# Kernel optimization log

Measured on AMD Instinct MI355X. Metric: run time of the kernel, lower is better.

## Reference

```python
import jax, jax.numpy as jnp
import numpy as np

L = 8192   # sequence length
B = 4      # batch
D = 512    # embed_dim
NDIM = 16  # EMA state dim
Z = 128    # shared q/k dim
W = 128    # attention window
MP = 256   # max relative positions
NEG = -50000.0  # TOKEN_SELF_ATTN_VALUE-style mask fill


def setup_inputs() -> dict:
    key = jax.random.key(0)
    ks = jax.random.split(key, 16)
    def tn(k, shp, std):  # truncated-normal-ish init (clipped normal)
        return jnp.clip(jax.random.normal(k, shp) * std, -2 * std, 2 * std)
    val = jnp.ones((NDIM, 1)).at[1::2].set(-1.0)  # MultiHeadEMA beta init pattern
    return {
        "x": jax.random.normal(ks[0], (L, B, D), dtype=jnp.float32),
        "delta": tn(ks[1], (D, NDIM, 1), 0.2),
        "alpha": tn(ks[2], (D, NDIM, 1), 0.2),
        "beta": tn(ks[3], (D, NDIM, 1), 0.02) + val,
        "gamma": jax.random.normal(ks[4], (D, NDIM)),
        "omega": jax.random.normal(ks[5], (D,)),
        "Wp": tn(ks[6], (D, 1), 0.02),      # LatentConfigurator weight_proj
        "bp": jnp.zeros((1,)),
        "temp": jnp.array([0.5 * np.log(D)], dtype=jnp.float32),  # log(sqrt(D))
        "Wz": tn(ks[7], (D, Z), 0.02),
        "qg": jax.random.normal(ks[8], (Z,)) * 0.02 + 1.0,
        "qb": jnp.zeros((Z,)),
        "kg": jax.random.normal(ks[9], (Z,)) * 0.02 + 1.0,
        "kb": jnp.zeros((Z,)),
        "Wv": tn(ks[10], (D, D), 0.02),
        "relb": tn(ks[11], (2 * MP - 1,), 0.02),  # FastRelativePositionalBias table
    }


def _rotary(t, cos, sin):
    # t: (B, L, Z); cos/sin: (L, Z//2). Complex rotation on interleaved pairs.
    t1, t2 = t[..., 0::2], t[..., 1::2]
    return jnp.stack([t1 * cos - t2 * sin, t1 * sin + t2 * cos], axis=-1).reshape(t.shape)


def _forward(x, delta, alpha, beta, gamma, omega, Wp, bp, temp, Wz, qg, qb, kg, kb, Wv, relb):
    scale = 1.0 / np.sqrt(NDIM)
    # ---- MultiHeadEMA: damped EMA as long convolution via FFT ----
    p = jax.nn.sigmoid(delta)                      # (D,N,1)
    a = jax.nn.sigmoid(alpha)
    logq = jnp.log1p(-(p * a))                     # log(1 - p*alpha)
    t = jnp.arange(L, dtype=jnp.float32)
    kern = (p * beta) * jnp.exp(logq * t)          # (D,N,L) Vandermonde kernel
    k1d = jnp.einsum('dnl,dn->dl', kern, gamma * scale)  # (D,L)
    xb = x.transpose(1, 2, 0)                      # (B,D,L)
    conv = jnp.fft.irfft(jnp.fft.rfft(xb, n=2 * L) * jnp.fft.rfft(k1d, n=2 * L), n=2 * L)[..., :L]
    mx = jax.nn.silu(conv.transpose(2, 0, 1) + x * omega)  # (L,B,D)
    # ---- LatentConfigurator: sigmoid token routing (proj_dim==1) ----
    pi = jax.nn.sigmoid((mx @ Wp + bp) / jnp.exp(temp))[..., 0].T  # (B,L)
    mxb = mx.transpose(1, 0, 2)                    # (B,L,D)
    sel = pi > 0.5
    idx = jnp.cumsum(sel.astype(jnp.int32), axis=1) * sel  # (B,L); 0 -> dropped slot
    counts = sel.sum(axis=1)                       # (B,)
    bi = jnp.arange(B)[:, None]
    # compress_seq: scatter selected tokens to compact prefix (slot 0 dropped)
    c = jnp.zeros((B, L + 1, D), mx.dtype).at[bi, idx].add(mxb * sel[..., None])[:, 1:]
    # ---- windowed attention over compressed tokens ----
    z = jax.nn.silu(c @ Wz)                        # (B,L,Z)
    freqs = 1.0 / (10000.0 ** (jnp.arange(0, Z, 2, dtype=jnp.float32) / Z))
    ang = jnp.arange(L, dtype=jnp.float32)[:, None] * freqs
    cos, sin = jnp.cos(ang), jnp.sin(ang)
    q = _rotary(z * qg + qb, cos, sin)
    kk = _rotary(z * kg + kb, cos, sin)
    v = jax.nn.silu(c @ Wv)                        # (B,L,D)
    n = L // W
    qw = q.reshape(B, n, W, Z)
    def look_around(tw):  # prepend previous window: (B,n,W,f) -> (B,n,2W,f)
        prev = jnp.pad(tw, ((0, 0), (1, 0), (0, 0), (0, 0)))[:, :-1]
        return jnp.concatenate([prev, tw], axis=2)
    kw = look_around(kk.reshape(B, n, W, Z))
    vw = look_around(v.reshape(B, n, W, D))
    base = (jnp.arange(n) * W)[:, None, None]
    qabs = base + jnp.arange(W)[None, :, None]         # (n,W,1)
    kabs = base + jnp.arange(-W, W)[None, None, :]     # (n,1,2W)
    mask = (kabs <= qabs) & (kabs >= 0) & (kabs[None] < counts[:, None, None, None])  # (B,n,W,2W)
    rel = jnp.arange(-W, W)[None, :] - jnp.arange(W)[:, None]   # (W,2W)
    bias = relb[jnp.clip(rel + MP - 1, 0, 2 * MP - 2)]          # (W,2W)
    scores = jnp.einsum('bnwz,bnkz->bnwk', qw, kw) / np.sqrt(Z) + bias
    attn = jax.nn.softmax(jnp.where(mask, scores, NEG), axis=-1)
    h = jnp.einsum('bnwk,bnkd->bnwd', attn, vw).reshape(B, L, D)
    # ---- extract: gather back to original positions, gate by pi ----
    hpad = jnp.concatenate([jnp.zeros((B, 1, D), h.dtype), h], axis=1)
    hsel = jnp.take_along_axis(hpad, idx[..., None], axis=1)    # (B,L,D)
    return x + (hsel * pi[..., None]).transpose(1, 0, 2)        # (L,B,D)


def reference(x, delta, alpha, beta, gamma, omega, Wp, bp, temp, Wz, qg, qb, kg, kb, Wv, relb):
    return _forward(x, delta, alpha, beta, gamma, omega, Wp, bp, temp, Wz, qg, qb, kg, kb, Wv, relb)
```

## Files before the change

### kernel.cpp

```cpp
#include <hip/hip_runtime.h>
#include <math.h>

constexpr int L = 8192;
constexpr int B = 4;
constexpr int D = 512;
constexpr int NDIM = 16;
constexpr int Z = 128;
constexpr float NEGF = -50000.0f;
constexpr int CCL = 64;
constexpr int NCH = L / CCL;
constexpr int FMAX = 64;

typedef short s16x8 __attribute__((ext_vector_type(8)));
typedef float f32x4 __attribute__((ext_vector_type(4)));

typedef __attribute__((address_space(1))) const void* as1cv;
typedef __attribute__((address_space(3))) void* as3v;

__device__ __forceinline__ void gld16(const void* g, void* l) {
  __builtin_amdgcn_global_load_lds((as1cv)g, (as3v)l, 16, 0, 0);
}

__device__ __forceinline__ unsigned short f2bf(float f) {
  unsigned u = __builtin_bit_cast(unsigned, f);
  u += 0x7fffu + ((u >> 16) & 1u);
  return (unsigned short)(u >> 16);
}

#define DPPADD(acc, ctrl, rmask)                                                   \
  {                                                                                \
    int _mv = __builtin_amdgcn_update_dpp(0, __builtin_bit_cast(int, acc),         \
                                          ctrl, rmask, 0xf, false);                \
    acc += __builtin_bit_cast(float, _mv);                                         \
  }

__global__ __launch_bounds__(256) void k_prep(const float* __restrict__ delta,
                                              const float* __restrict__ alpha,
                                              const float* __restrict__ beta,
                                              const float* __restrict__ gamma,
                                              double* __restrict__ qdn,
                                              double* __restrict__ cdn,
                                              double* __restrict__ rp1,
                                              double* __restrict__ rp2,
                                              float* __restrict__ qf,
                                              float* __restrict__ cf,
                                              float* __restrict__ r1f,
                                              float* __restrict__ r2f,
                                              int* __restrict__ fcnt) {
  int i = blockIdx.x * 256 + threadIdx.x;
  if (i == 0) *fcnt = 0;
  if (i >= D * NDIM) return;
  double p = 1.0 / (1.0 + exp(-(double)delta[i]));
  double a = 1.0 / (1.0 + exp(-(double)alpha[i]));
  double q = 1.0 - p * a;
  double c = p * (double)beta[i] * (double)gamma[i] * 0.25;
  qdn[i] = q; cdn[i] = c;
  double q2 = q * q, q4 = q2 * q2, q8 = q4 * q4;
  double q16 = q8 * q8, q32 = q16 * q16, q64 = q32 * q32;
  rp1[i] = q64;
  rp2[i] = q64 * q64;
  qf[i] = (float)q; cf[i] = (float)c;
  r1f[i] = (float)q64; r2f[i] = (float)(q64 * q64);
}

__global__ __launch_bounds__(256) void k_tab(float2* __restrict__ tab) {
  int tid = blockIdx.x * 256 + threadIdx.x;
  int i = tid & 63, j = tid >> 6;
  double freq = exp(((double)(-2 * i) / 128.0) * log(10000.0));
  float angf = (float)j * (float)freq;
  double sa, ca;
  sincos((double)angf, &sa, &ca);
  float2 r; r.x = (float)ca; r.y = (float)sa;
  tab[tid] = r;
}

__global__ __launch_bounds__(256) void k_convA(const float* __restrict__ x,
                                               const float* __restrict__ qf,
                                               float* __restrict__ E) {
  int bx = blockIdx.x;
  int tile = bx & 31, dg = (bx >> 5) & 7, b = bx >> 8;
  int dl = threadIdx.x & 63, cl = threadIdx.x >> 6;
  int dgl = dg * 64 + dl;
  int t = tile * 4 + cl;
  float q[NDIM], s[NDIM];
#pragma unroll
  for (int n = 0; n < NDIM; ++n) { q[n] = qf[dgl * NDIM + n]; s[n] = 0.f; }
  const float* xp = x + ((size_t)(t * CCL) * B + b) * D + dgl;
#pragma unroll 4
  for (int i = 0; i < CCL; ++i) {
    float xv = xp[i * (B * D)];
#pragma unroll
    for (int n = 0; n < NDIM; ++n) s[n] = fmaf(q[n], s[n], xv);
  }
  float* eb = E + ((size_t)(b * NCH + t) * NDIM) * 512 + dgl;
#pragma unroll
  for (int n = 0; n < NDIM; ++n) eb[(size_t)n * 512] = s[n];
}

__global__ __launch_bounds__(256) void k_convC(const float* __restrict__ x,
                                               const float* __restrict__ omega,
                                               const float* __restrict__ qf,
                                               const float* __restrict__ cf,
                                               const float* __restrict__ r1f,
                                               const float* __restrict__ r2f,
                                               const float* __restrict__ E,
                                               const float* __restrict__ Wp,
                                               unsigned short* __restrict__ mxb,
                                               float* __restrict__ pdot) {
  int bx = blockIdx.x;
  int tile = bx & 31, dg = (bx >> 5) & 7, b = bx >> 8;
  int dl = threadIdx.x & 63, cl = threadIdx.x >> 6;
  int dgl = dg * 64 + dl;
  int t = tile * 4 + cl;
  float q[NDIM], c[NDIM], s[NDIM];
#pragma unroll
  for (int n = 0; n < NDIM; ++n) {
    q[n] = qf[dgl * NDIM + n];
    c[n] = cf[dgl * NDIM + n];
    s[n] = 0.f;
  }
  if (t >= 1) {
    const float* e1 = E + ((size_t)(b * NCH + t - 1) * NDIM) * 512 + dgl;
#pragma unroll
    for (int n = 0; n < NDIM; ++n) s[n] = e1[(size_t)n * 512];
  }
  if (t >= 2) {
    const float* e2 = E + ((size_t)(b * NCH + t - 2) * NDIM) * 512 + dgl;
#pragma unroll
    for (int n = 0; n < NDIM; ++n) s[n] = fmaf(r1f[dgl * NDIM + n], e2[(size_t)n * 512], s[n]);
  }
  if (t >= 3) {
    const float* e3 = E + ((size_t)(b * NCH + t - 3) * NDIM) * 512 + dgl;
#pragma unroll
    for (int n = 0; n < NDIM; ++n) s[n] = fmaf(r2f[dgl * NDIM + n], e3[(size_t)n * 512], s[n]);
  }
  float om = omega[dgl];
  float wp = Wp[dgl];
  const float* xp = x + ((size_t)(t * CCL) * B + b) * D + dgl;
  unsigned short* mp = mxb + ((size_t)b * L + t * CCL) * 512 + dgl;
  float* pp = pdot + ((size_t)(b * L + t * CCL)) * 8 + dg;
#pragma unroll 4
  for (int i = 0; i < CCL; ++i) {
    float xv = xp[i * (B * D)];
#pragma unroll
    for (int n = 0; n < NDIM; ++n) s[n] = fmaf(q[n], s[n], xv);
    float p0 = c[0] * s[0], p1 = c[1] * s[1], p2 = c[2] * s[2], p3 = c[3] * s[3];
    p0 = fmaf(c[4], s[4], p0);  p1 = fmaf(c[5], s[5], p1);
    p2 = fmaf(c[6], s[6], p2);  p3 = fmaf(c[7], s[7], p3);
    p0 = fmaf(c[8], s[8], p0);  p1 = fmaf(c[9], s[9], p1);
    p2 = fmaf(c[10], s[10], p2); p3 = fmaf(c[11], s[11], p3);
    p0 = fmaf(c[12], s[12], p0); p1 = fmaf(c[13], s[13], p1);
    p2 = fmaf(c[14], s[14], p2); p3 = fmaf(c[15], s[15], p3);
    float conv = (p0 + p1) + (p2 + p3);
    float m = fmaf(xv, om, conv);
    float v = m / (1.0f + __expf(-m));
    mp[(size_t)i * 512] = f2bf(v);
    float pd = v * wp;
    DPPADD(pd, 0x111, 0xf);
    DPPADD(pd, 0x112, 0xf);
    DPPADD(pd, 0x114, 0xf);
    DPPADD(pd, 0x118, 0xf);
    DPPADD(pd, 0x142, 0xa);
    DPPADD(pd, 0x143, 0x8);
    if (dl == 63) pp[(size_t)i * 8] = pd;
  }
}

__global__ __launch_bounds__(256) void k_logitc(const float* __restrict__ pdot,
                                                const float* __restrict__ bp,
                                                const float* __restrict__ temp,
                                                float* __restrict__ pi,
                                                int* __restrict__ selb,
                                                int* __restrict__ fcnt,
                                                int* __restrict__ flags) {
  int rid = blockIdx.x * 256 + threadIdx.x;
  const float* pr = pdot + (size_t)rid * 8;
  double acc = 0.0;
#pragma unroll
  for (int j = 0; j < 8; ++j) acc += (double)pr[j];
  double logit = acc + (double)bp[0];
  pi[rid] = (float)(1.0 / (1.0 + exp(-logit / exp((double)temp[0]))));
  selb[rid] = (logit > 0.0) ? 1 : 0;
  if (fabs(logit) < 1e-4) {
    int slot = atomicAdd(fcnt, 1);
    if (slot < FMAX) flags[slot] = rid;
  }
}

__global__ __launch_bounds__(256) void k_fix(const int* __restrict__ fcnt,
                                             const int* __restrict__ flags,
                                             const float* __restrict__ x,
                                             const double* __restrict__ qdn,
                                             const double* __restrict__ cdn,
                                             const double* __restrict__ rp1,
                                             const double* __restrict__ rp2,
                                             const float* __restrict__ omega,
                                             const float* __restrict__ Wp,
                                             double* __restrict__ pfix) {
  int nb = blockIdx.x;
  int fi = nb >> 3, dblk = nb & 7;
  int count = *fcnt; if (count > FMAX) count = FMAX;
  if (fi >= count) return;
  int rid = flags[fi];
  int b = rid >> 13, l = rid & (L - 1);
  int t = l >> 6, io = l & 63;
  int sub = threadIdx.x >> 6, dl = threadIdx.x & 63;
  int d = dblk * 64 + dl;
  double q[NDIM], s[NDIM];
#pragma unroll
  for (int n = 0; n < NDIM; ++n) { q[n] = qdn[d * NDIM + n]; s[n] = 0.0; }
  int c0 = (sub < 3) ? (t - 3 + sub) : t;
  int steps = (sub < 3) ? 64 : (io + 1);
  if (c0 >= 0) {
    const float* xp = x + ((size_t)(c0 * CCL) * B + b) * D + d;
    for (int i = 0; i < steps; ++i) {
      double xv = (double)xp[(size_t)i * (B * D)];
#pragma unroll
      for (int n = 0; n < NDIM; ++n) s[n] = fma(q[n], s[n], xv);
    }
  }
  __shared__ double Esm[4][64][NDIM];
#pragma unroll
  for (int n = 0; n < NDIM; ++n) Esm[sub][dl][n] = s[n];
  __syncthreads();
  if (sub == 3) {
    double sfin[NDIM];
#pragma unroll
    for (int n = 0; n < NDIM; ++n) {
      double base = q[n], r = 1.0;
      int e = io + 1;
      while (e) { if (e & 1) r *= base; base *= base; e >>= 1; }
      double S = Esm[2][dl][n] + rp1[d * NDIM + n] * Esm[1][dl][n] + rp2[d * NDIM + n] * Esm[0][dl][n];
      sfin[n] = Esm[3][dl][n] + r * S;
    }
    double conv = 0.0;
#pragma unroll
    for (int n = 0; n < NDIM; ++n) conv = fma(cdn[d * NDIM + n], sfin[n], conv);
    double xv = (double)x[((size_t)l * B + b) * D + d];
    double m = conv + xv * (double)omega[d];
    double mxd = m / (1.0 + exp(-m));
    double v = mxd * (double)Wp[d];
#pragma unroll
    for (int off = 32; off; off >>= 1) v += __shfl_down(v, off, 64);
    if (dl == 0) pfix[fi * 8 + dblk] = v;
  }
}

__global__ __launch_bounds__(64) void k_fix2(const int* __restrict__ fcnt,
                                             const int* __restrict__ flags,
                                             const double* __restrict__ pfix,
                                             const float* __restrict__ bp,
                                             const float* __restrict__ temp,
                                             float* __restrict__ pi,
                                             int* __restrict__ selb) {
  int fi = threadIdx.x;
  int count = *fcnt; if (count > FMAX) count = FMAX;
  if (fi >= count) return;
  double s = 0.0;
#pragma unroll
  for (int j = 0; j < 8; ++j) s += pfix[fi * 8 + j];
  double logit = s + (double)bp[0];
  int rid = flags[fi];
  selb[rid] = (logit > 0.0) ? 1 : 0;
  pi[rid] = (float)(1.0 / (1.0 + exp(-logit / exp((double)temp[0]))));
}

__global__ __launch_bounds__(256) void k_scan(const int* __restrict__ selb,
                                              int* __restrict__ idx,
                                              int* __restrict__ src,
                                              int* __restrict__ counts) {
  int b = blockIdx.x;
  int t = threadIdx.x;
  __shared__ int part[256];
  const int PER = L / 256;
  int base = b * L + t * PER;
  int loc[PER];
  int cnt = 0;
#pragma unroll
  for (int i = 0; i < PER; ++i) { loc[i] = selb[base + i]; cnt += loc[i]; }
  part[t] = cnt;
  __syncthreads();
  for (int off = 1; off < 256; off <<= 1) {
    int v = (t >= off) ? part[t - off] : 0;
    __syncthreads();
    part[t] += v;
    __syncthreads();
  }
  int run = (t == 0) ? 0 : part[t - 1];
#pragma unroll
  for (int i = 0; i < PER; ++i) {
    int sflag = loc[i];
    run += sflag;
    idx[base + i] = sflag ? run : 0;
    if (sflag) src[b * L + run - 1] = t * PER + i;
  }
  if (t == 255) counts[b] = part[255];
  __syncthreads();
  int total = part[255];
  for (int i2 = total + t; i2 < L; i2 += 256) src[b * L + i2] = 0;
}

__global__ __launch_bounds__(256) void k_wt(const float* __restrict__ Wm,
                                            unsigned short* __restrict__ Wt, int N) {
  int idx = blockIdx.x * 256 + threadIdx.x;
  int n = idx >> 9, kk = idx & 511;
  Wt[idx] = f2bf(Wm[(size_t)kk * N + n]);
}

__global__ __launch_bounds__(256) void k_gemm_mfma(const unsigned short* __restrict__ mxb,
                                                   const int* __restrict__ src,
                                                   const unsigned short* __restrict__ Bt,
                                                   float* __restrict__ outF,
                                                   unsigned short* __restrict__ outT,
                                                   int N, int mode) {
  __shared__ char smem[32768];
  char* As = smem;
  char* Bs = smem + 16384;
  int tid = threadIdx.x;
  int w = tid >> 6, l = tid & 63;
  int m0 = blockIdx.x * 128, n0 = blockIdx.y * 128;
  int gb = m0 >> 13, j0 = m0 & 8191;
  int wr = w >> 1, wc = w & 1;
  const unsigned short* arow[4];
  const unsigned short* brow[4];
#pragma unroll
  for (int ld = 0; ld < 4; ++ld) {
    int li = w * 4 + ld;
    int row = li * 8 + (l >> 3);
    int col = ((l & 7) ^ (row & 7)) << 3;
    int srow = src[gb * 8192 + j0 + row];
    arow[ld] = mxb + ((size_t)gb * 8192 + srow) * 512 + col;
    brow[ld] = Bt + (size_t)(n0 + row) * 512 + col;
  }
  f32x4 acc[4][4];
  f32x4 zz = {0.f, 0.f, 0.f, 0.f};
#pragma unroll
  for (int mi = 0; mi < 4; ++mi)
#pragma unroll
    for (int ni = 0; ni < 4; ++ni) acc[mi][ni] = zz;

  for (int k0 = 0; k0 < 512; k0 += 64) {
#pragma unroll
    for (int ld = 0; ld < 4; ++ld) {
      int li = w * 4 + ld;
      gld16(arow[ld] + k0, As + li * 1024);
      gld16(brow[ld] + k0, Bs + li * 1024);
    }
    __syncthreads();
    s16x8 af[4][2], bfr[4][2];
#pragma unroll
    for (int kh = 0; kh < 2; ++kh) {
#pragma unroll
      for (int mi = 0; mi < 4; ++mi) {
        int row = wr * 64 + mi * 16 + (l & 15);
        int byte = row * 128 + ((kh * 64 + ((l >> 4) * 16)) ^ ((row & 7) << 4));
        af[mi][kh] = *(const s16x8*)(As + byte);
      }
#pragma unroll
      for (int ni = 0; ni < 4; ++ni) {
        int row = wc * 64 + ni * 16 + (l & 15);
        int byte = row * 128 + ((kh * 64 + ((l >> 4) * 16)) ^ ((row & 7) << 4));
        bfr[ni][kh] = *(const s16x8*)(Bs + byte);
      }
    }
#pragma unroll
    for (int kh = 0; kh < 2; ++kh)
#pragma unroll
      for (int mi = 0; mi < 4; ++mi)
#pragma unroll
        for (int ni = 0; ni < 4; ++ni)
          acc[mi][ni] = __builtin_amdgcn_mfma_f32_16x16x32_bf16(af[mi][kh], bfr[ni][kh], acc[mi][ni], 0, 0, 0);
    __syncthreads();
  }
  if (mode == 0) {
#pragma unroll
    for (int mi = 0; mi < 4; ++mi)
#pragma unroll
      for (int ni = 0; ni < 4; ++ni)
#pragma unroll
        for (int r = 0; r < 4; ++r) {
          float vv = acc[mi][ni][r];
          vv = vv / (1.0f + __expf(-vv));
          int mrow = m0 + wr * 64 + mi * 16 + (l >> 4) * 4 + r;
          int ncol = n0 + wc * 64 + ni * 16 + (l & 15);
          outF[(size_t)mrow * N + ncol] = vv;
        }
  } else {
    unsigned short* ts = (unsigned short*)smem;
    (void)ts;
#pragma unroll
    for (int mi = 0; mi < 4; ++mi)
#pragma unroll
      for (int ni = 0; ni < 4; ++ni)
#pragma unroll
        for (int r = 0; r < 4; ++r) {
          float vv = acc[mi][ni][r];
          vv = vv / (1.0f + __expf(-vv));
          int mrow = wr * 64 + mi * 16 + (l >> 4) * 4 + r;
          int ncol = wc * 64 + ni * 16 + (l & 15);
          int byteoff = ncol * 256 + ((mrow * 2) ^ ((ncol & 7) << 4));
          *(unsigned short*)(smem + byteoff) = f2bf(vv);
        }
    __syncthreads();
#pragma unroll
    for (int it = 0; it < 8; ++it) {
      int ncol = w * 32 + it * 4 + (l >> 4);
      int ch = l & 15;
      int byteoff = ncol * 256 + ((ch * 16) ^ ((ncol & 7) << 4));
      s16x8 vch = *(const s16x8*)(smem + byteoff);
      *(s16x8*)(outT + ((size_t)(gb * 512 + n0 + ncol)) * 8192 + j0 + ch * 8) = vch;
    }
  }
}

__global__ __launch_bounds__(256) void k_rot(const float* __restrict__ z,
                                             const float2* __restrict__ tab,
                                             const float* __restrict__ qg,
                                             const float* __restrict__ qb,
                                             const float* __restrict__ kg,
                                             const float* __restrict__ kb,
                                             unsigned short* __restrict__ qo,
                                             unsigned short* __restrict__ ko) {
  int tid = blockIdx.x * 256 + threadIdx.x;
  int i = tid & 63;
  int row = tid >> 6;
  int j = row & (L - 1);
  float2 cs = tab[j * 64 + i];
  float cc = cs.x, ss = cs.y;
  size_t base = (size_t)row * Z + 2 * i;
  float z1 = z[base], z2 = z[base + 1];
  float q1 = z1 * qg[2 * i] + qb[2 * i], q2 = z2 * qg[2 * i + 1] + qb[2 * i + 1];
  float k1 = z1 * kg[2 * i] + kb[2 * i], k2 = z2 * kg[2 * i + 1] + kb[2 * i + 1];
  qo[base]     = f2bf(q1 * cc - q2 * ss);
  qo[base + 1] = f2bf(q1 * ss + q2 * cc);
  ko[base]     = f2bf(k1 * cc - k2 * ss);
  ko[base + 1] = f2bf(k1 * ss + k2 * cc);
}

__global__ __launch_bounds__(512) void k_attn_mfma(const unsigned short* __restrict__ q,
                                                   const unsigned short* __restrict__ k,
                                                   const unsigned short* __restrict__ vT,
                                                   const float* __restrict__ relb,
                                                   const int* __restrict__ counts,
                                                   float* __restrict__ h) {
  __shared__ char smem[131072];
  char* Qs = smem;
  char* Ks = smem + 32768;
  char* Ps = smem;
  char* Vs = smem + 65536;
  int tid = threadIdx.x, w = tid >> 6, l = tid & 63;
  int n = blockIdx.x & 63, b = blockIdx.x >> 6;
  int cnt = counts[b];
  int q0 = n * 128, kbase = q0 - 128;
  const size_t rowb = (size_t)b * L;

#pragma unroll
  for (int ld = 0; ld < 4; ++ld) {
    int li = w * 4 + ld;
    int row = li * 4 + (l >> 4);
    int colb = ((l & 15) * 16) ^ ((row & 7) << 4);
    gld16((const char*)(q + (rowb + q0 + row) * Z) + colb, Qs + li * 1024);
  }
#pragma unroll
  for (int ld = 0; ld < 8; ++ld) {
    int li = w * 8 + ld;
    int row = li * 4 + (l >> 4);
    int jk = kbase + row; if (jk < 0) jk = 0;
    int colb = ((l & 15) * 16) ^ ((row & 7) << 4);
    gld16((const char*)(k + (rowb + jk) * Z) + colb, Ks + li * 1024);
  }
  __syncthreads();

  int m0 = w * 16;
  f32x4 s[16];
  f32x4 zz = {0.f, 0.f, 0.f, 0.f};
#pragma unroll
  for (int ni = 0; ni < 16; ++ni) s[ni] = zz;
  s16x8 aq[4];
#pragma unroll
  for (int ks = 0; ks < 4; ++ks) {
    int row = m0 + (l & 15);
    int byte = row * 256 + ((ks * 64 + ((l >> 4) * 16)) ^ ((row & 7) << 4));
    aq[ks] = *(const s16x8*)(Qs + byte);
  }
#pragma unroll
  for (int ni = 0; ni < 16; ++ni) {
    int row = ni * 16 + (l & 15);
    int rb = row * 256, sw = (row & 7) << 4;
#pragma unroll
    for (int ks = 0; ks < 4; ++ks) {
      s16x8 bk = *(const s16x8*)(Ks + rb + ((ks * 64 + ((l >> 4) * 16)) ^ sw));
      s[ni] = __builtin_amdgcn_mfma_f32_16x16x32_bf16(aq[ks], bk, s[ni], 0, 0, 0);
    }
  }
  __syncthreads();

  auto stageV = [&](int nc) {
#pragma unroll
    for (int ld = 0; ld < 8; ++ld) {
      int li = w * 8 + ld;
      int row = li * 2 + (l >> 5);
      int colb = ((l & 31) * 16) ^ ((row & 7) << 4);
      int j = kbase + (colb >> 1);
      if (j < 0) j = 0;
      gld16((const char*)(vT + ((size_t)(b * 512 + nc * 128 + row)) * L + j), Vs + li * 1024);
    }
  };
  stageV(0);

  int rgrp = (l >> 4) * 4;
  float mxr[4] = {-3e38f, -3e38f, -3e38f, -3e38f};
#pragma unroll
  for (int ni = 0; ni < 16; ++ni) {
    int col = ni * 16 + (l & 15);
    int kabs = kbase + col;
#pragma unroll
    for (int r = 0; r < 4; ++r) {
      int ww = m0 + rgrp + r;
      bool valid = (kabs >= 0) && (kabs <= q0 + ww) && (kabs < cnt);
      float vv = valid ? (s[ni][r] * 0.08838834764831845f + relb[col + 127 - ww]) : NEGF;
      s[ni][r] = vv;
      mxr[r] = fmaxf(mxr[r], vv);
    }
  }
#pragma unroll
  for (int r = 0; r < 4; ++r)
    for (int off = 1; off < 16; off <<= 1)
      mxr[r] = fmaxf(mxr[r], __shfl_xor(mxr[r], off, 64));
  float smr[4] = {0.f, 0.f, 0.f, 0.f};
#pragma unroll
  for (int ni = 0; ni < 16; ++ni)
#pragma unroll
    for (int r = 0; r < 4; ++r) {
      float p = __expf(s[ni][r] - mxr[r]);
      s[ni][r] = p;
      smr[r] += p;
    }
#pragma unroll
  for (int r = 0; r < 4; ++r) {
    for (int off = 1; off < 16; off <<= 1) smr[r] += __shfl_xor(smr[r], off, 64);
    smr[r] = 1.0f / smr[r];
  }
#pragma unroll
  for (int ni = 0; ni < 16; ++ni) {
    int colb2 = (ni * 16 + (l & 15)) * 2;
#pragma unroll
    for (int r = 0; r < 4; ++r) {
      int row = m0 + rgrp + r;
      *(unsigned short*)(Ps + row * 512 + (colb2 ^ ((row & 7) << 4))) = f2bf(s[ni][r] * smr[r]);
    }
  }
  __syncthreads();

  for (int nc = 0; nc < 4; ++nc) {
    if (nc) {
      __syncthreads();
      stageV(nc);
      __syncthreads();
    }
    f32x4 o[8];
#pragma unroll
    for (int ni = 0; ni < 8; ++ni) o[ni] = zz;
    int prow = m0 + (l & 15);
    int psw = (prow & 7) << 4;
#pragma unroll
    for (int kt = 0; kt < 4; ++kt) {
      s16x8 pa0 = *(const s16x8*)(Ps + prow * 512 + ((kt * 128 + ((l >> 4) * 16)) ^ psw));
      s16x8 pa1 = *(const s16x8*)(Ps + prow * 512 + ((kt * 128 + 64 + ((l >> 4) * 16)) ^ psw));
#pragma unroll
      for (int ni = 0; ni < 8; ++ni) {
        int vrow = ni * 16 + (l & 15);
        int vsw = (vrow & 7) << 4;
        s16x8 vb0 = *(const s16x8*)(Vs + vrow * 512 + ((kt * 128 + ((l >> 4) * 16)) ^ vsw));
        s16x8 vb1 = *(const s16x8*)(Vs + vrow * 512 + ((kt * 128 + 64 + ((l >> 4) * 16)) ^ vsw));
        o[ni] = __builtin_amdgcn_mfma_f32_16x16x32_bf16(pa0, vb0, o[ni], 0, 0, 0);
        o[ni] = __builtin_amdgcn_mfma_f32_16x16x32_bf16(pa1, vb1, o[ni], 0, 0, 0);
      }
    }
#pragma unroll
    for (int ni = 0; ni < 8; ++ni)
#pragma unroll
      for (int r = 0; r < 4; ++r)
        h[(rowb + q0 + m0 + rgrp + r) * 512 + nc * 128 + ni * 16 + (l & 15)] = o[ni][r];
  }
}

__global__ __launch_bounds__(256) void k_final(const float* __restrict__ x,
                                               const float* __restrict__ h,
                                               const float* __restrict__ pi,
                                               const int* __restrict__ idx,
                                               float* __restrict__ out) {
  int e4 = blockIdx.x * 256 + threadIdx.x;
  int dq = e4 & 127;
  int rem = e4 >> 7;
  int b = rem & 3;
  int l = rem >> 2;
  float4 xv = ((const float4*)x)[e4];
  int ix = idx[(b << 13) + l];
  if (ix > 0) {
    float pv = pi[(b << 13) + l];
    float4 hv = ((const float4*)(h + ((size_t)(b << 13) + ix - 1) * 512))[dq];
    xv.x += hv.x * pv; xv.y += hv.y * pv;
    xv.z += hv.z * pv; xv.w += hv.w * pv;
  }
  ((float4*)out)[e4] = xv;
}

extern "C" void kernel_launch(void* const* d_in, const int* in_sizes, int n_in,
                              void* d_out, int out_size, void* d_ws, size_t ws_size,
                              hipStream_t stream) {
  const float* x     = (const float*)d_in[0];
  const float* delta = (const float*)d_in[1];
  const float* alpha = (const float*)d_in[2];
  const float* beta  = (const float*)d_in[3];
  const float* gamma = (const float*)d_in[4];
  const float* omega = (const float*)d_in[5];
  const float* Wp    = (const float*)d_in[6];
  const float* bp    = (const float*)d_in[7];
  const float* temp  = (const float*)d_in[8];
  const float* Wz    = (const float*)d_in[9];
  const float* qg    = (const float*)d_in[10];
  const float* qb    = (const float*)d_in[11];
  const float* kg    = (const float*)d_in[12];
  const float* kb    = (const float*)d_in[13];
  const float* Wv    = (const float*)d_in[14];
  const float* relb  = (const float*)d_in[15];
  (void)in_sizes; (void)n_in; (void)out_size; (void)ws_size;

  char* wsb = (char*)d_ws;
  size_t o = 0;
  auto alloc = [&](size_t bytes) {
    char* p = wsb + o;
    o += (bytes + 255) & ~(size_t)255;
    return p;
  };
  float* hbuf          = (float*)alloc((size_t)B * L * D * 4);
  unsigned short* mxb  = (unsigned short*)hbuf;
  float* Ebuf          = (float*)((char*)hbuf + (size_t)B * L * D * 2);
  float* zb            = (float*)alloc((size_t)B * L * Z * 4);
  unsigned short* qb2  = (unsigned short*)alloc((size_t)B * L * Z * 2);
  unsigned short* kb2  = (unsigned short*)alloc((size_t)B * L * Z * 2);
  unsigned short* vTb  = (unsigned short*)alloc((size_t)B * D * L * 2);
  unsigned short* wzt  = (unsigned short*)alloc((size_t)Z * 512 * 2);
  unsigned short* wvt  = (unsigned short*)alloc((size_t)D * 512 * 2);
  float2* tab = (float2*)alloc((size_t)L * 64 * 8);
  float* pdot = (float*)alloc((size_t)B * L * 8 * 4);
  float* pib  = (float*)alloc((size_t)B * L * 4);
  int* selb   = (int*)alloc((size_t)B * L * 4);
  int* idx    = (int*)alloc((size_t)B * L * 4);
  int* src    = (int*)alloc((size_t)B * L * 4);
  int* cnt    = (int*)alloc(256);
  double* qdn = (double*)alloc((size_t)D * NDIM * 8);
  double* cdn = (double*)alloc((size_t)D * NDIM * 8);
  double* rp1 = (double*)alloc((size_t)D * NDIM * 8);
  double* rp2 = (double*)alloc((size_t)D * NDIM * 8);
  float* qf   = (float*)alloc((size_t)D * NDIM * 4);
  float* cf   = (float*)alloc((size_t)D * NDIM * 4);
  float* r1f  = (float*)alloc((size_t)D * NDIM * 4);
  float* r2f  = (float*)alloc((size_t)D * NDIM * 4);
  int* fcnt   = (int*)alloc(256);
  int* flags  = (int*)alloc(FMAX * 4);
  double* pfix = (double*)alloc((size_t)FMAX * 8 * 8);

  k_prep<<<(D * NDIM + 255) / 256, 256, 0, stream>>>(delta, alpha, beta, gamma,
                                                     qdn, cdn, rp1, rp2, qf, cf, r1f, r2f, fcnt);
  k_tab<<<L * 64 / 256, 256, 0, stream>>>(tab);
  k_convA<<<B * 8 * 32, 256, 0, stream>>>(x, qf, Ebuf);
  k_convC<<<B * 8 * 32, 256, 0, stream>>>(x, omega, qf, cf, r1f, r2f, Ebuf, Wp, mxb, pdot);
  k_logitc<<<B * L / 256, 256, 0, stream>>>(pdot, bp, temp, pib, selb, fcnt, flags);
  k_fix<<<FMAX * 8, 256, 0, stream>>>(fcnt, flags, x, qdn, cdn, rp1, rp2, omega, Wp, pfix);
  k_fix2<<<1, 64, 0, stream>>>(fcnt, flags, pfix, bp, temp, pib, selb);
  k_scan<<<B, 256, 0, stream>>>(selb, idx, src, cnt);
  k_wt<<<Z * 512 / 256, 256, 0, stream>>>(Wz, wzt, Z);
  k_wt<<<D * 512 / 256, 256, 0, stream>>>(Wv, wvt, D);
  k_gemm_mfma<<<dim3(256, 1), 256, 0, stream>>>(mxb, src, wzt, zb, vTb, Z, 0);
  k_gemm_mfma<<<dim3(256, 4), 256, 0, stream>>>(mxb, src, wvt, zb, vTb, D, 1);
  k_rot<<<B * L * (Z / 2) / 256, 256, 0, stream>>>(zb, tab, qg, qb, kg, kb, qb2, kb2);
  k_attn_mfma<<<B * 64, 512, 0, stream>>>(qb2, kb2, vTb, relb, cnt, hbuf);
  k_final<<<(int)((size_t)L * B * D / 4 / 256), 256, 0, stream>>>(x, hbuf, pib, idx, (float*)d_out);
}
```

Baseline: 230.2 us.

## Fuse gather-gate-residual epilogue into attention and batch x loads in EMA conv

The attention kernel now scatters its output straight to the original positions, computing x + h*pi in place. A small fill kernel copies x only for unselected rows, so the fp32 h buffer round trip and the separate final pass are gone. The EMA conv kernels now load 32 x values up front before the recurrence to expose memory-level parallelism, and the value GEMM remaps blocks so tiles sharing A rows land on the same XCD. The costs are higher register pressure in the conv kernels and scattered, uncoalesced row writes from attention.

Measured after the change: 229.3 us. Within noise of the previous version (-0.4%).

```diff
diff --git a/kernel.cpp b/kernel.cpp
--- a/kernel.cpp
+++ b/kernel.cpp
@@ -86,11 +86,16 @@
 #pragma unroll
   for (int n = 0; n < NDIM; ++n) { q[n] = qf[dgl * NDIM + n]; s[n] = 0.f; }
   const float* xp = x + ((size_t)(t * CCL) * B + b) * D + dgl;
-#pragma unroll 4
-  for (int i = 0; i < CCL; ++i) {
-    float xv = xp[i * (B * D)];
-#pragma unroll
-    for (int n = 0; n < NDIM; ++n) s[n] = fmaf(q[n], s[n], xv);
+#pragma unroll
+  for (int ii = 0; ii < CCL; ii += 32) {
+    float xv[32];
+#pragma unroll
+    for (int u = 0; u < 32; ++u) xv[u] = xp[(ii + u) * (B * D)];
+#pragma unroll
+    for (int u = 0; u < 32; ++u) {
+#pragma unroll
+      for (int n = 0; n < NDIM; ++n) s[n] = fmaf(q[n], s[n], xv[u]);
+    }
   }
   float* eb = E + ((size_t)(b * NCH + t) * NDIM) * 512 + dgl;
 #pragma unroll
@@ -139,30 +144,36 @@
   const float* xp = x + ((size_t)(t * CCL) * B + b) * D + dgl;
   unsigned short* mp = mxb + ((size_t)b * L + t * CCL) * 512 + dgl;
   float* pp = pdot + ((size_t)(b * L + t * CCL)) * 8 + dg;
-#pragma unroll 4
-  for (int i = 0; i < CCL; ++i) {
-    float xv = xp[i * (B * D)];
-#pragma unroll
-    for (int n = 0; n < NDIM; ++n) s[n] = fmaf(q[n], s[n], xv);
-    float p0 = c[0] * s[0], p1 = c[1] * s[1], p2 = c[2] * s[2], p3 = c[3] * s[3];
-    p0 = fmaf(c[4], s[4], p0);  p1 = fmaf(c[5], s[5], p1);
-    p2 = fmaf(c[6], s[6], p2);  p3 = fmaf(c[7], s[7], p3);
-    p0 = fmaf(c[8], s[8], p0);  p1 = fmaf(c[9], s[9], p1);
-    p2 = fmaf(c[10], s[10], p2); p3 = fmaf(c[11], s[11], p3);
-    p0 = fmaf(c[12], s[12], p0); p1 = fmaf(c[13], s[13], p1);
-    p2 = fmaf(c[14], s[14], p2); p3 = fmaf(c[15], s[15], p3);
-    float conv = (p0 + p1) + (p2 + p3);
-    float m = fmaf(xv, om, conv);
-    float v = m / (1.0f + __expf(-m));
-    mp[(size_t)i * 512] = f2bf(v);
-    float pd = v * wp;
-    DPPADD(pd, 0x111, 0xf);
-    DPPADD(pd, 0x112, 0xf);
-    DPPADD(pd, 0x114, 0xf);
-    DPPADD(pd, 0x118, 0xf);
-    DPPADD(pd, 0x142, 0xa);
-    DPPADD(pd, 0x143, 0x8);
-    if (dl == 63) pp[(size_t)i * 8] = pd;
+#pragma unroll
+  for (int ii = 0; ii < CCL; ii += 32) {
+    float xv[32];
+#pragma unroll
+    for (int u = 0; u < 32; ++u) xv[u] = xp[(ii + u) * (B * D)];
+#pragma unroll
+    for (int u = 0; u < 32; ++u) {
+      int i = ii + u;
+#pragma unroll
+      for (int n = 0; n < NDIM; ++n) s[n] = fmaf(q[n], s[n], xv[u]);
+      float p0 = c[0] * s[0], p1 = c[1] * s[1], p2 = c[2] * s[2], p3 = c[3] * s[3];
+      p0 = fmaf(c[4], s[4], p0);  p1 = fmaf(c[5], s[5], p1);
+      p2 = fmaf(c[6], s[6], p2);  p3 = fmaf(c[7], s[7], p3);
+      p0 = fmaf(c[8], s[8], p0);  p1 = fmaf(c[9], s[9], p1);
+      p2 = fmaf(c[10], s[10], p2); p3 = fmaf(c[11], s[11], p3);
+      p0 = fmaf(c[12], s[12], p0); p1 = fmaf(c[13], s[13], p1);
+      p2 = fmaf(c[14], s[14], p2); p3 = fmaf(c[15], s[15], p3);
+      float conv = (p0 + p1) + (p2 + p3);
+      float m = fmaf(xv[u], om, conv);
+      float v = m / (1.0f + __expf(-m));
+      mp[(size_t)i * 512] = f2bf(v);
+      float pd = v * wp;
+      DPPADD(pd, 0x111, 0xf);
+      DPPADD(pd, 0x112, 0xf);
+      DPPADD(pd, 0x114, 0xf);
+      DPPADD(pd, 0x118, 0xf);
+      DPPADD(pd, 0x142, 0xa);
+      DPPADD(pd, 0x143, 0x8);
+      if (dl == 63) pp[(size_t)i * 8] = pd;
+    }
   }
 }
 
@@ -318,7 +329,16 @@
   char* Bs = smem + 16384;
   int tid = threadIdx.x;
   int w = tid >> 6, l = tid & 63;
-  int m0 = blockIdx.x * 128, n0 = blockIdx.y * 128;
+  int mtile, ntile;
+  if (mode == 1) {
+    int lin = blockIdx.y * 256 + blockIdx.x;
+    int xcd = lin & 7, loc = lin >> 3;
+    mtile = xcd * 32 + (loc >> 2);
+    ntile = loc & 3;
+  } else {
+    mtile = blockIdx.x; ntile = blockIdx.y;
+  }
+  int m0 = mtile * 128, n0 = ntile * 128;
   int gb = m0 >> 13, j0 = m0 & 8191;
   int wr = w >> 1, wc = w & 1;
   const unsigned short* arow[4];
@@ -386,8 +406,6 @@
           outF[(size_t)mrow * N + ncol] = vv;
         }
   } else {
-    unsigned short* ts = (unsigned short*)smem;
-    (void)ts;
 #pragma unroll
     for (int mi = 0; mi < 4; ++mi)
 #pragma unroll
@@ -442,7 +460,10 @@
                                                    const unsigned short* __restrict__ vT,
                                                    const float* __restrict__ relb,
                                                    const int* __restrict__ counts,
-                                                   float* __restrict__ h) {
+                                                   const int* __restrict__ src,
+                                                   const float* __restrict__ pi,
+                                                   const float* __restrict__ x,
+                                                   float* __restrict__ out) {
   __shared__ char smem[131072];
   char* Qs = smem;
   char* Ks = smem + 32768;
@@ -552,6 +573,16 @@
   }
   __syncthreads();
 
+  int tlr[4]; float pvr[4]; bool vr[4];
+#pragma unroll
+  for (int r = 0; r < 4; ++r) {
+    int jq = q0 + m0 + rgrp + r;
+    vr[r] = (jq < cnt);
+    int tl = vr[r] ? src[(b << 13) + jq] : 0;
+    tlr[r] = tl;
+    pvr[r] = pi[(b << 13) + tl];
+  }
+
   for (int nc = 0; nc < 4; ++nc) {
     if (nc) {
       __syncthreads();
@@ -581,29 +612,22 @@
     for (int ni = 0; ni < 8; ++ni)
 #pragma unroll
       for (int r = 0; r < 4; ++r)
-        h[(rowb + q0 + m0 + rgrp + r) * 512 + nc * 128 + ni * 16 + (l & 15)] = o[ni][r];
-  }
-}
-
-__global__ __launch_bounds__(256) void k_final(const float* __restrict__ x,
-                                               const float* __restrict__ h,
-                                               const float* __restrict__ pi,
-                                               const int* __restrict__ idx,
-                                               float* __restrict__ out) {
+        if (vr[r]) {
+          size_t off = ((size_t)tlr[r] * B + b) * 512 + nc * 128 + ni * 16 + (l & 15);
+          out[off] = fmaf(o[ni][r], pvr[r], x[off]);
+        }
+  }
+}
+
+__global__ __launch_bounds__(256) void k_fill(const float* __restrict__ x,
+                                              const int* __restrict__ idx,
+                                              float* __restrict__ out) {
   int e4 = blockIdx.x * 256 + threadIdx.x;
-  int dq = e4 & 127;
   int rem = e4 >> 7;
   int b = rem & 3;
   int l = rem >> 2;
-  float4 xv = ((const float4*)x)[e4];
-  int ix = idx[(b << 13) + l];
-  if (ix > 0) {
-    float pv = pi[(b << 13) + l];
-    float4 hv = ((const float4*)(h + ((size_t)(b << 13) + ix - 1) * 512))[dq];
-    xv.x += hv.x * pv; xv.y += hv.y * pv;
-    xv.z += hv.z * pv; xv.w += hv.w * pv;
-  }
-  ((float4*)out)[e4] = xv;
+  if (idx[(b << 13) + l] == 0)
+    ((float4*)out)[e4] = ((const float4*)x)[e4];
 }
 
 extern "C" void kernel_launch(void* const* d_in, const int* in_sizes, int n_in,
@@ -634,9 +658,8 @@
     o += (bytes + 255) & ~(size_t)255;
     return p;
   };
-  float* hbuf          = (float*)alloc((size_t)B * L * D * 4);
-  unsigned short* mxb  = (unsigned short*)hbuf;
-  float* Ebuf          = (float*)((char*)hbuf + (size_t)B * L * D * 2);
+  unsigned short* mxb  = (unsigned short*)alloc((size_t)B * L * D * 4);
+  float* Ebuf          = (float*)((char*)mxb + (size_t)B * L * D * 2);
   float* zb            = (float*)alloc((size_t)B * L * Z * 4);
   unsigned short* qb2  = (unsigned short*)alloc((size_t)B * L * Z * 2);
   unsigned short* kb2  = (unsigned short*)alloc((size_t)B * L * Z * 2);
@@ -676,6 +699,6 @@
   k_gemm_mfma<<<dim3(256, 1), 256, 0, stream>>>(mxb, src, wzt, zb, vTb, Z, 0);
   k_gemm_mfma<<<dim3(256, 4), 256, 0, stream>>>(mxb, src, wvt, zb, vTb, D, 1);
   k_rot<<<B * L * (Z / 2) / 256, 256, 0, stream>>>(zb, tab, qg, qb, kg, kb, qb2, kb2);
-  k_attn_mfma<<<B * 64, 512, 0, stream>>>(qb2, kb2, vTb, relb, cnt, hbuf);
-  k_final<<<(int)((size_t)L * B * D / 4 / 256), 256, 0, stream>>>(x, hbuf, pib, idx, (float*)d_out);
-}
+  k_fill<<<(int)((size_t)L * B * D / 4 / 256), 256, 0, stream>>>(x, idx, (float*)d_out);
+  k_attn_mfma<<<B * 64, 512, 0, stream>>>(qb2, kb2, vTb, relb, cnt, src, pib, x, (float*)d_out);
+}
```
